# Kernel optimization log

Measured on AMD Instinct MI355X. Metric: run time of the kernel, lower is better.

Reference implementation:

```python
import jax, jax.numpy as jnp
import numpy as np
import math

B, S, D, H = 2, 2048, 1024, 16

def setup_inputs() -> dict:
    key = jax.random.key(0)
    ks = jax.random.split(key, 13)
    def lin(kw, kb, out_d, in_d):
        W = jax.random.normal(kw, (out_d, in_d), dtype=jnp.float32) * 0.02
        b = jax.random.normal(kb, (out_d,), dtype=jnp.float32) * 0.02
        return W, b
    Wq, bq = lin(ks[0], ks[1], D, D)
    Wk, bk = lin(ks[2], ks[3], D, D)
    Wv, bv = lin(ks[4], ks[5], D, D)
    Wo, bo = lin(ks[6], ks[7], D, D)
    query = jax.random.normal(ks[8], (B, S, D), dtype=jnp.float32)
    key_t = jax.random.normal(ks[9], (B, S, D), dtype=jnp.float32)
    value = jax.random.normal(ks[10], (B, S, D), dtype=jnp.float32)
    src_mask = jax.random.randint(ks[11], (B, S), 0, 2).astype(bool)  # True = masked out
    return {"query": query, "key": key_t, "value": value, "src_mask": src_mask,
            "Wq": Wq, "bq": bq, "Wk": Wk, "bk": bk, "Wv": Wv, "bv": bv,
            "Wo": Wo, "bo": bo, "nhead": H}

def reference(query, key, value, src_mask, Wq, bq, Wk, bk, Wv, bv, Wo, bo, nhead):
    b, s, d = query.shape
    hd = d // nhead
    scale = 1.0 / math.sqrt(hd)
    def split_heads(x):  # [b,s,d] -> [b,h,s,hd]
        return x.reshape(b, -1, nhead, hd).transpose(0, 2, 1, 3)
    q = split_heads(query @ Wq.T + bq)
    k = split_heads(key @ Wk.T + bk)
    v = split_heads(value @ Wv.T + bv)
    scores = jnp.einsum('bhqe,bhke->bhqk', q, k) * scale  # [b,h,s,s]
    # mask True -> -9e9, broadcast over heads and query positions (matches repeat)
    scores = jnp.where(src_mask[:, None, None, :], jnp.float32(-9e9), scores)
    probs = jax.nn.softmax(scores, axis=-1)
    # dropout is identity in eval mode
    out = jnp.einsum('bhqk,bhke->bhqe', probs, v)  # [b,h,s,hd]
    out = out.transpose(0, 2, 1, 3).reshape(b, s, d)
    out = out @ Wo.T + bo
    return out
```

## Files before the change

### kernel.cpp

```cpp
#include <hip/hip_runtime.h>
#include <hip/hip_bf16.h>
#include <cstdint>
#include <cstddef>

#define B_ 2
#define S_ 2048
#define D_ 1024
#define H_ 16
#define HD_ 64
#define M_ 4096

typedef __attribute__((ext_vector_type(8))) short short8;
typedef __attribute__((ext_vector_type(4))) float floatx4;
typedef __attribute__((ext_vector_type(16))) float f32x16;
typedef __attribute__((ext_vector_type(2))) int intx2;

__device__ __forceinline__ floatx4 mfma32(short8 a, short8 b, floatx4 c) {
    return __builtin_amdgcn_mfma_f32_16x16x32_bf16(a, b, c, 0, 0, 0);
}
__device__ __forceinline__ f32x16 mfma3216(short8 a, short8 b, f32x16 c) {
    return __builtin_amdgcn_mfma_f32_32x32x16_bf16(a, b, c, 0, 0, 0);
}

__device__ __forceinline__ void gload_lds16(const __hip_bfloat16* g, __hip_bfloat16* lds_base) {
    __builtin_amdgcn_global_load_lds(
        (const __attribute__((address_space(1))) void*)g,
        (__attribute__((address_space(3))) void*)lds_base, 16, 0, 0);
}

__device__ __forceinline__ int pkbf(float a, float b) {
    union { __hip_bfloat162 h; int i; } u;
    u.h = __float22bfloat162_rn({a, b});
    return u.i;
}
__device__ __forceinline__ void pl32swap(int& a, int& b) {
    intx2 r = __builtin_amdgcn_permlane32_swap(a, b, false, false);
    a = r.x; b = r.y;
}

__global__ __launch_bounds__(256) void cvt_all_kernel(
    const float* __restrict__ q, const float* __restrict__ k, const float* __restrict__ v,
    const float* __restrict__ wq, const float* __restrict__ wk,
    const float* __restrict__ wv, const float* __restrict__ wo,
    const int* __restrict__ mask,
    __hip_bfloat16* __restrict__ dstIn,
    __hip_bfloat16* __restrict__ dstW,
    float* __restrict__ fbias)
{
    const int bid = blockIdx.x;
    const int tid = threadIdx.x;
    const size_t SZ_IN = (size_t)M_ * D_;
    const size_t SZ_W  = (size_t)D_ * D_;
    if (bid < 12288) {
        int z = bid >> 12, xb = bid & 4095;
        const float* src = z == 0 ? q : z == 1 ? k : v;
        __hip_bfloat16* d = dstIn + (size_t)z * SZ_IN;
        int i = (xb * 256 + tid) * 4;
        float4 val = *(const float4*)(src + i);
        union { __hip_bfloat16 h[4]; uint2 u; } cv;
        cv.h[0] = __float2bfloat16(val.x); cv.h[1] = __float2bfloat16(val.y);
        cv.h[2] = __float2bfloat16(val.z); cv.h[3] = __float2bfloat16(val.w);
        *(uint2*)(d + i) = cv.u;
    } else if (bid < 16384) {
        int r  = bid - 12288;
        int z  = r >> 10, xb = r & 1023;
        const float* src = z == 0 ? wq : z == 1 ? wk : z == 2 ? wv : wo;
        __hip_bfloat16* d = dstW + (size_t)z * SZ_W;
        int i = (xb * 256 + tid) * 4;
        float4 val = *(const float4*)(src + i);
        union { __hip_bfloat16 h[4]; uint2 u; } cv;
        cv.h[0] = __float2bfloat16(val.x); cv.h[1] = __float2bfloat16(val.y);
        cv.h[2] = __float2bfloat16(val.z); cv.h[3] = __float2bfloat16(val.w);
        *(uint2*)(d + i) = cv.u;
    } else {
        int i = ((bid - 16384) * 256 + tid) * 4;
        int4 m = *(const int4*)(mask + i);
        float4 o;
        o.x = m.x ? -100000.0f : 0.0f;
        o.y = m.y ? -100000.0f : 0.0f;
        o.z = m.z ? -100000.0f : 0.0f;
        o.w = m.w ? -100000.0f : 0.0f;
        *(float4*)(fbias + i) = o;
    }
}

template <int MODE>
__device__ __forceinline__ void gemm_core(
    const __hip_bfloat16* __restrict__ A,
    const __hip_bfloat16* __restrict__ W,
    const float* __restrict__ bias,
    void* __restrict__ Cout,
    __hip_bfloat16* __restrict__ smem,
    int m0, int n0, int N)
{
    __hip_bfloat16* As = smem;
    __hip_bfloat16* Bs = smem + 128 * 32;
    const int K = D_;
    const int tid  = threadIdx.x;
    const int wave = tid >> 6;
    const int lane = tid & 63;
    const int quad = lane >> 4;
    const int l15  = lane & 15;
    const int wm   = (wave & 1) * 64;
    const int wn   = (wave >> 1) * 64;
    const int srow = lane >> 2;
    const int scol = (lane & 3) * 8;

    floatx4 acc[4][4];
#pragma unroll
    for (int i = 0; i < 4; i++)
#pragma unroll
        for (int j = 0; j < 4; j++) {
            floatx4 z = {0.f, 0.f, 0.f, 0.f};
            acc[i][j] = z;
        }

    for (int k0 = 0; k0 < K; k0 += 32) {
        __syncthreads();
#pragma unroll
        for (int t = 0; t < 2; t++) {
            int r0 = wave * 32 + t * 16;
            gload_lds16(A + (size_t)(m0 + r0 + srow) * K + k0 + scol, As + r0 * 32);
            gload_lds16(W + (size_t)(n0 + r0 + srow) * K + k0 + scol, Bs + r0 * 32);
        }
        __syncthreads();

        short8 afr[4], bfr[4];
#pragma unroll
        for (int i = 0; i < 4; i++)
            afr[i] = *(const short8*)(As + (wm + i * 16 + l15) * 32 + quad * 8);
#pragma unroll
        for (int j = 0; j < 4; j++)
            bfr[j] = *(const short8*)(Bs + (wn + j * 16 + l15) * 32 + quad * 8);
#pragma unroll
        for (int i = 0; i < 4; i++)
#pragma unroll
            for (int j = 0; j < 4; j++)
                acc[i][j] = mfma32(afr[i], bfr[j], acc[i][j]);
    }

    if constexpr (MODE == 1) {
#pragma unroll
        for (int j = 0; j < 4; j++) {
            int col = n0 + wn + j * 16 + l15;
            int h = col >> 6, e = col & 63;
            float bv = bias[col];
#pragma unroll
            for (int i = 0; i < 4; i++) {
                int s0 = m0 + wm + i * 16 + quad * 4;
                int bb = s0 >> 11, sl = s0 & 2047;
                union { __hip_bfloat16 hx[4]; uint2 u; } pk;
#pragma unroll
                for (int r = 0; r < 4; r++)
                    pk.hx[r] = __float2bfloat16(acc[i][j][r] + bv);
                *(uint2*)((__hip_bfloat16*)Cout + (((size_t)bb * H_ + h) * HD_ + e) * S_ + sl) = pk.u;
            }
        }
    } else {
#pragma unroll
        for (int j = 0; j < 4; j++) {
            int col = n0 + wn + j * 16 + l15;
            float bv = bias[col];
#pragma unroll
            for (int i = 0; i < 4; i++) {
#pragma unroll
                for (int r = 0; r < 4; r++) {
                    int rowg = m0 + wm + i * 16 + quad * 4 + r;
                    ((__hip_bfloat16*)Cout)[(size_t)rowg * N + col] =
                        __float2bfloat16(acc[i][j][r] + bv);
                }
            }
        }
    }
}

__global__ __launch_bounds__(256) void qkv_gemm_kernel(
    const __hip_bfloat16* __restrict__ qb, const __hip_bfloat16* __restrict__ kb,
    const __hip_bfloat16* __restrict__ vb,
    const __hip_bfloat16* __restrict__ Wqb, const __hip_bfloat16* __restrict__ Wkb,
    const __hip_bfloat16* __restrict__ Wvb,
    const float* __restrict__ bq, const float* __restrict__ bk, const float* __restrict__ bv,
    __hip_bfloat16* __restrict__ Qp, __hip_bfloat16* __restrict__ Kp,
    __hip_bfloat16* __restrict__ Vt)
{
    __shared__ __hip_bfloat16 smem[2 * 128 * 32] __attribute__((aligned(16)));
    const int z = blockIdx.z;
    const __hip_bfloat16* A = z == 0 ? qb : z == 1 ? kb : vb;
    const __hip_bfloat16* W = z == 0 ? Wqb : z == 1 ? Wkb : Wvb;
    const float* bias = z == 0 ? bq : z == 1 ? bk : bv;
    int m0 = blockIdx.y * 128, n0 = blockIdx.x * 128;
    if (z < 2) gemm_core<0>(A, W, bias, z == 0 ? (void*)Qp : (void*)Kp, smem, m0, n0, D_);
    else       gemm_core<1>(A, W, bias, (void*)Vt, smem, m0, n0, D_);
}

__global__ __launch_bounds__(256) void oproj_gemm_kernel(
    const __hip_bfloat16* __restrict__ A, const __hip_bfloat16* __restrict__ W,
    const float* __restrict__ bias, float* __restrict__ out)
{
    __shared__ __hip_bfloat16 As[64 * 32]  __attribute__((aligned(16)));
    __shared__ __hip_bfloat16 Bs[128 * 32] __attribute__((aligned(16)));
    const int K = D_, N = D_;
    const int tid  = threadIdx.x;
    const int m0   = blockIdx.y * 64;
    const int n0   = blockIdx.x * 128;
    const int wave = tid >> 6;
    const int lane = tid & 63;
    const int quad = lane >> 4;
    const int l15  = lane & 15;
    const int wm   = (wave & 1) * 32;
    const int wn   = (wave >> 1) * 64;
    const int srow = lane >> 2;
    const int scol = (lane & 3) * 8;

    floatx4 acc[2][4];
#pragma unroll
    for (int i = 0; i < 2; i++)
#pragma unroll
        for (int j = 0; j < 4; j++) {
            floatx4 z = {0.f, 0.f, 0.f, 0.f};
            acc[i][j] = z;
        }

    for (int k0 = 0; k0 < K; k0 += 32) {
        __syncthreads();
        {
            int ra = wave * 16;
            gload_lds16(A + (size_t)(m0 + ra + srow) * K + k0 + scol, As + ra * 32);
#pragma unroll
            for (int t = 0; t < 2; t++) {
                int rb = wave * 32 + t * 16;
                gload_lds16(W + (size_t)(n0 + rb + srow) * K + k0 + scol, Bs + rb * 32);
            }
        }
        __syncthreads();

        short8 afr[2], bfr[4];
#pragma unroll
        for (int i = 0; i < 2; i++)
            afr[i] = *(const short8*)(As + (wm + i * 16 + l15) * 32 + quad * 8);
#pragma unroll
        for (int j = 0; j < 4; j++)
            bfr[j] = *(const short8*)(Bs + (wn + j * 16 + l15) * 32 + quad * 8);
#pragma unroll
        for (int i = 0; i < 2; i++)
#pragma unroll
            for (int j = 0; j < 4; j++)
                acc[i][j] = mfma32(afr[i], bfr[j], acc[i][j]);
    }

#pragma unroll
    for (int j = 0; j < 4; j++) {
        int col = n0 + wn + j * 16 + l15;
        float bv = bias[col];
#pragma unroll
        for (int i = 0; i < 2; i++) {
#pragma unroll
            for (int r = 0; r < 4; r++) {
                int rowg = m0 + wm + i * 16 + quad * 4 + r;
                out[(size_t)rowg * N + col] = acc[i][j][r] + bv;
            }
        }
    }
}

#define LDP 72
#define NT_ (S_ / 64)
__global__ __launch_bounds__(256, 2) void flash_attn_kernel(
    const __hip_bfloat16* __restrict__ Q,
    const __hip_bfloat16* __restrict__ Kp,
    const __hip_bfloat16* __restrict__ Vt,
    const float* __restrict__ fbias,
    __hip_bfloat16* __restrict__ O)
{
    __shared__ __hip_bfloat16 Qs  [128 * LDP]    __attribute__((aligned(16)));
    __shared__ __hip_bfloat16 KsB [2][64 * LDP]  __attribute__((aligned(16)));
    __shared__ __hip_bfloat16 VtsB[2][64 * LDP]  __attribute__((aligned(16)));

    const int tid  = threadIdx.x;
    const int q0   = blockIdx.x * 128;
    const int bh   = blockIdx.y;
    const int b    = bh >> 4;
    const int h    = bh & 15;
    const int warp = tid >> 6;
    const int lane = tid & 63;
    const int l31  = lane & 31;
    const int hi   = lane >> 5;
    const float kSc = 0.18033688f;

    const size_t baseQ = ((size_t)b * S_ + q0) * D_ + (size_t)h * HD_;
#pragma unroll
    for (int c = tid; c < 1024; c += 256) {
        int row = c >> 3, kc = c & 7;
        *(uint4*)(Qs + row * LDP + kc * 8) = *(const uint4*)(Q + baseQ + (size_t)row * D_ + kc * 8);
    }

    const float* brow = fbias + b * S_;
    const __hip_bfloat16* VtBase = Vt + (size_t)bh * HD_ * S_;
    const size_t baseKrow = (size_t)b * S_ * D_ + (size_t)h * HD_;

    const int r0  = tid >> 3;
    const int kc0 = (tid & 7) * 8;

    uint4 kreg[2], vreg[2];
    auto issue = [&](int kv0) {
#pragma unroll
        for (int i = 0; i < 2; i++) {
            kreg[i] = *(const uint4*)(Kp + baseKrow + (size_t)(kv0 + r0 + 32 * i) * D_ + kc0);
            vreg[i] = *(const uint4*)(VtBase + (size_t)(r0 + 32 * i) * S_ + kv0 + kc0);
        }
    };
    auto commit = [&](int pb) {
#pragma unroll
        for (int i = 0; i < 2; i++) {
            *(uint4*)(KsB[pb]  + (r0 + 32 * i) * LDP + kc0) = kreg[i];
            *(uint4*)(VtsB[pb] + (r0 + 32 * i) * LDP + kc0) = vreg[i];
        }
    };

    issue(0);
    commit(0);
    __syncthreads();

    short8 qb[4];
#pragma unroll
    for (int ks = 0; ks < 4; ks++)
        qb[ks] = *(const short8*)(Qs + (warp * 32 + l31) * LDP + ks * 16 + hi * 8);

    float lsum = 0.f;
    f32x16 o_acc[2];
#pragma unroll
    for (int hdb = 0; hdb < 2; hdb++)
#pragma unroll
        for (int r = 0; r < 16; r++) o_acc[hdb][r] = 0.f;

    for (int t = 0; t < NT_; ++t) {
        if (t) __syncthreads();

        floatx4 brg[2][4];
#pragma unroll
        for (int kvb = 0; kvb < 2; kvb++)
#pragma unroll
            for (int g = 0; g < 4; g++)
                brg[kvb][g] = *(const floatx4*)(brow + t * 64 + kvb * 32 + g * 8 + hi * 4);

        if (t + 1 < NT_) issue((t + 1) * 64);

        const __hip_bfloat16* Ks  = KsB [t & 1];
        const __hip_bfloat16* Vts = VtsB[t & 1];

        f32x16 s_acc[2];
        __builtin_amdgcn_s_setprio(1);
#pragma unroll
        for (int kvb = 0; kvb < 2; kvb++) {
            f32x16 z;
#pragma unroll
            for (int r = 0; r < 16; r++) z[r] = 0.f;
#pragma unroll
            for (int ks = 0; ks < 4; ks++) {
                short8 ka = *(const short8*)(Ks + (kvb * 32 + l31) * LDP + ks * 16 + hi * 8);
                z = mfma3216(ka, qb[ks], z);
            }
            s_acc[kvb] = z;
        }
        __builtin_amdgcn_s_setprio(0);

        short8 pa[4];
#pragma unroll
        for (int kvb = 0; kvb < 2; kvb++) {
            float p[16];
#pragma unroll
            for (int r = 0; r < 16; r++)
                p[r] = __builtin_amdgcn_exp2f(s_acc[kvb][r] * kSc + brg[kvb][r >> 2][r & 3]);
#pragma unroll
            for (int r = 0; r < 16; r += 4)
                lsum += (p[r] + p[r + 1]) + (p[r + 2] + p[r + 3]);
#pragma unroll
            for (int ksl = 0; ksl < 2; ksl++) {
                int pb = ksl * 8;
                int w0 = pkbf(p[pb + 0], p[pb + 1]);
                int w2 = pkbf(p[pb + 4], p[pb + 5]);
                int w1 = pkbf(p[pb + 2], p[pb + 3]);
                int w3 = pkbf(p[pb + 6], p[pb + 7]);
                pl32swap(w0, w2);
                pl32swap(w1, w3);
                union { int w[4]; short8 s; } fr;
                fr.w[0] = w0; fr.w[1] = w1; fr.w[2] = w2; fr.w[3] = w3;
                pa[kvb * 2 + ksl] = fr.s;
            }
        }

        __builtin_amdgcn_s_setprio(1);
#pragma unroll
        for (int hdb = 0; hdb < 2; hdb++)
#pragma unroll
            for (int ks = 0; ks < 4; ks++) {
                short8 vb = *(const short8*)(Vts + (hdb * 32 + l31) * LDP + ks * 16 + hi * 8);
                o_acc[hdb] = mfma3216(pa[ks], vb, o_acc[hdb]);
            }
        __builtin_amdgcn_s_setprio(0);

        if (t + 1 < NT_) commit((t + 1) & 1);
    }

    lsum += __shfl_xor(lsum, 32);
    float inv = 1.0f / lsum;

    const size_t baseO = ((size_t)b * S_ + q0 + warp * 32) * D_ + (size_t)h * HD_;
#pragma unroll
    for (int r = 0; r < 16; r++) {
        int crow = (r & 3) + 8 * (r >> 2) + 4 * hi;
        float iv = __shfl(inv, crow);
#pragma unroll
        for (int hdb = 0; hdb < 2; hdb++)
            O[baseO + (size_t)crow * D_ + hdb * 32 + l31] =
                __float2bfloat16(o_acc[hdb][r] * iv);
    }
}

extern "C" void kernel_launch(void* const* d_in, const int* in_sizes, int n_in,
                              void* d_out, int out_size, void* d_ws, size_t ws_size,
                              hipStream_t stream) {
    const float* query = (const float*)d_in[0];
    const float* key   = (const float*)d_in[1];
    const float* value = (const float*)d_in[2];
    const int*   mask  = (const int*)d_in[3];
    const float* Wq    = (const float*)d_in[4];
    const float* bq    = (const float*)d_in[5];
    const float* Wk    = (const float*)d_in[6];
    const float* bk    = (const float*)d_in[7];
    const float* Wv    = (const float*)d_in[8];
    const float* bv    = (const float*)d_in[9];
    const float* Wo    = (const float*)d_in[10];
    const float* bo    = (const float*)d_in[11];
    float* out = (float*)d_out;

    const size_t SZ_IN = (size_t)M_ * D_;
    const size_t SZ_W  = (size_t)D_ * D_;
    __hip_bfloat16* qb  = (__hip_bfloat16*)d_ws;
    __hip_bfloat16* kb  = qb  + SZ_IN;
    __hip_bfloat16* vb  = kb  + SZ_IN;
    __hip_bfloat16* Wqb = vb  + SZ_IN;
    __hip_bfloat16* Wkb = Wqb + SZ_W;
    __hip_bfloat16* Wvb = Wkb + SZ_W;
    __hip_bfloat16* Wob = Wvb + SZ_W;
    __hip_bfloat16* Qp  = Wob + SZ_W;
    __hip_bfloat16* Kp  = Qp  + SZ_IN;
    __hip_bfloat16* Vt  = Kp  + SZ_IN;
    float*          fb  = (float*)(Vt + SZ_IN);

    cvt_all_kernel<<<dim3(16388), 256, 0, stream>>>(
        query, key, value, Wq, Wk, Wv, Wo, mask, qb, Wqb, fb);

    qkv_gemm_kernel<<<dim3(D_ / 128, M_ / 128, 3), 256, 0, stream>>>(
        qb, kb, vb, Wqb, Wkb, Wvb, bq, bk, bv, Qp, Kp, Vt);

    flash_attn_kernel<<<dim3(S_ / 128, B_ * H_), 256, 0, stream>>>(Qp, Kp, Vt, fb, Qp);

    oproj_gemm_kernel<<<dim3(D_ / 128, M_ / 64), 256, 0, stream>>>(Qp, Wob, bo, out);
}
```

Before: 249.4 us.

## Split each KV tile across two warp groups in flash attention

The attention kernel now runs 512 threads per block. Two groups of four warps each take one 32-key half of every 64-key tile and keep their own partial output and row-sum accumulators. The halves are combined through shared memory at the end, and the Q, K and V staging is folded into one shared buffer that is reused for that reduction. The aim is more resident waves and shorter per-warp dependency chains to hide latency. In exchange it adds an epilogue reduction, and the tighter launch bounds raise register pressure and the risk of spills.

Result: faster. 229.5 us (-8.0%).

```diff
diff --git a/kernel.cpp b/kernel.cpp
--- a/kernel.cpp
+++ b/kernel.cpp
@@ -264,17 +264,16 @@
 }
 
 #define LDP 72
-#define NT_ (S_ / 64)
-__global__ __launch_bounds__(256, 2) void flash_attn_kernel(
+#define NTK (S_ / 64)
+#define KVBUF (64 * LDP)
+__global__ __launch_bounds__(512, 4) void flash_attn_kernel(
     const __hip_bfloat16* __restrict__ Q,
     const __hip_bfloat16* __restrict__ Kp,
     const __hip_bfloat16* __restrict__ Vt,
     const float* __restrict__ fbias,
     __hip_bfloat16* __restrict__ O)
 {
-    __shared__ __hip_bfloat16 Qs  [128 * LDP]    __attribute__((aligned(16)));
-    __shared__ __hip_bfloat16 KsB [2][64 * LDP]  __attribute__((aligned(16)));
-    __shared__ __hip_bfloat16 VtsB[2][64 * LDP]  __attribute__((aligned(16)));
+    __shared__ __hip_bfloat16 smem[4 * KVBUF] __attribute__((aligned(16)));
 
     const int tid  = threadIdx.x;
     const int q0   = blockIdx.x * 128;
@@ -282,6 +281,8 @@
     const int b    = bh >> 4;
     const int h    = bh & 15;
     const int warp = tid >> 6;
+    const int qw   = warp & 3;
+    const int kvh  = warp >> 2;
     const int lane = tid & 63;
     const int l31  = lane & 31;
     const int hi   = lane >> 5;
@@ -289,10 +290,17 @@
 
     const size_t baseQ = ((size_t)b * S_ + q0) * D_ + (size_t)h * HD_;
 #pragma unroll
-    for (int c = tid; c < 1024; c += 256) {
+    for (int c = tid; c < 1024; c += 512) {
         int row = c >> 3, kc = c & 7;
-        *(uint4*)(Qs + row * LDP + kc * 8) = *(const uint4*)(Q + baseQ + (size_t)row * D_ + kc * 8);
-    }
+        *(uint4*)(smem + row * LDP + kc * 8) =
+            *(const uint4*)(Q + baseQ + (size_t)row * D_ + kc * 8);
+    }
+    __syncthreads();
+    short8 qb[4];
+#pragma unroll
+    for (int ks = 0; ks < 4; ks++)
+        qb[ks] = *(const short8*)(smem + (qw * 32 + l31) * LDP + ks * 16 + hi * 8);
+    __syncthreads();
 
     const float* brow = fbias + b * S_;
     const __hip_bfloat16* VtBase = Vt + (size_t)bh * HD_ * S_;
@@ -301,31 +309,20 @@
     const int r0  = tid >> 3;
     const int kc0 = (tid & 7) * 8;
 
-    uint4 kreg[2], vreg[2];
+    uint4 kreg, vreg;
     auto issue = [&](int kv0) {
-#pragma unroll
-        for (int i = 0; i < 2; i++) {
-            kreg[i] = *(const uint4*)(Kp + baseKrow + (size_t)(kv0 + r0 + 32 * i) * D_ + kc0);
-            vreg[i] = *(const uint4*)(VtBase + (size_t)(r0 + 32 * i) * S_ + kv0 + kc0);
-        }
+        kreg = *(const uint4*)(Kp + baseKrow + (size_t)(kv0 + r0) * D_ + kc0);
+        vreg = *(const uint4*)(VtBase + (size_t)r0 * S_ + kv0 + kc0);
     };
     auto commit = [&](int pb) {
-#pragma unroll
-        for (int i = 0; i < 2; i++) {
-            *(uint4*)(KsB[pb]  + (r0 + 32 * i) * LDP + kc0) = kreg[i];
-            *(uint4*)(VtsB[pb] + (r0 + 32 * i) * LDP + kc0) = vreg[i];
-        }
+        *(uint4*)(smem + pb * KVBUF + r0 * LDP + kc0) = kreg;
+        *(uint4*)(smem + (2 + pb) * KVBUF + r0 * LDP + kc0) = vreg;
     };
 
     issue(0);
     commit(0);
     __syncthreads();
 
-    short8 qb[4];
-#pragma unroll
-    for (int ks = 0; ks < 4; ks++)
-        qb[ks] = *(const short8*)(Qs + (warp * 32 + l31) * LDP + ks * 16 + hi * 8);
-
     float lsum = 0.f;
     f32x16 o_acc[2];
 #pragma unroll
@@ -333,87 +330,95 @@
 #pragma unroll
         for (int r = 0; r < 16; r++) o_acc[hdb][r] = 0.f;
 
-    for (int t = 0; t < NT_; ++t) {
+    for (int t = 0; t < NTK; ++t) {
         if (t) __syncthreads();
 
-        floatx4 brg[2][4];
-#pragma unroll
-        for (int kvb = 0; kvb < 2; kvb++)
-#pragma unroll
-            for (int g = 0; g < 4; g++)
-                brg[kvb][g] = *(const floatx4*)(brow + t * 64 + kvb * 32 + g * 8 + hi * 4);
-
-        if (t + 1 < NT_) issue((t + 1) * 64);
-
-        const __hip_bfloat16* Ks  = KsB [t & 1];
-        const __hip_bfloat16* Vts = VtsB[t & 1];
-
-        f32x16 s_acc[2];
+        if (t + 1 < NTK) issue((t + 1) * 64);
+
+        const __hip_bfloat16* Ks  = smem + (t & 1) * KVBUF;
+        const __hip_bfloat16* Vts = smem + (2 + (t & 1)) * KVBUF;
+
+        f32x16 z;
+#pragma unroll
+        for (int r = 0; r < 16; r++) z[r] = 0.f;
         __builtin_amdgcn_s_setprio(1);
 #pragma unroll
-        for (int kvb = 0; kvb < 2; kvb++) {
-            f32x16 z;
-#pragma unroll
-            for (int r = 0; r < 16; r++) z[r] = 0.f;
-#pragma unroll
-            for (int ks = 0; ks < 4; ks++) {
-                short8 ka = *(const short8*)(Ks + (kvb * 32 + l31) * LDP + ks * 16 + hi * 8);
-                z = mfma3216(ka, qb[ks], z);
-            }
-            s_acc[kvb] = z;
+        for (int ks = 0; ks < 4; ks++) {
+            short8 ka = *(const short8*)(Ks + (kvh * 32 + l31) * LDP + ks * 16 + hi * 8);
+            z = mfma3216(ka, qb[ks], z);
         }
         __builtin_amdgcn_s_setprio(0);
 
-        short8 pa[4];
-#pragma unroll
-        for (int kvb = 0; kvb < 2; kvb++) {
-            float p[16];
+        short8 pa[2];
+#pragma unroll
+        for (int ksl = 0; ksl < 2; ksl++) {
+            const float* bb = brow + t * 64 + kvh * 32 + ksl * 16 + hi * 4;
+            floatx4 b0 = *(const floatx4*)(bb);
+            floatx4 b1 = *(const floatx4*)(bb + 8);
+            float p[8];
+#pragma unroll
+            for (int i = 0; i < 8; i++) {
+                float bias = (i < 4) ? b0[i & 3] : b1[i & 3];
+                p[i] = __builtin_amdgcn_exp2f(z[ksl * 8 + i] * kSc + bias);
+            }
+            lsum += ((p[0] + p[1]) + (p[2] + p[3])) + ((p[4] + p[5]) + (p[6] + p[7]));
+            int w0 = pkbf(p[0], p[1]);
+            int w2 = pkbf(p[4], p[5]);
+            int w1 = pkbf(p[2], p[3]);
+            int w3 = pkbf(p[6], p[7]);
+            pl32swap(w0, w2);
+            pl32swap(w1, w3);
+            union { int w[4]; short8 s; } fr;
+            fr.w[0] = w0; fr.w[1] = w1; fr.w[2] = w2; fr.w[3] = w3;
+            pa[ksl] = fr.s;
+        }
+
+        __builtin_amdgcn_s_setprio(1);
+#pragma unroll
+        for (int hdb = 0; hdb < 2; hdb++)
+#pragma unroll
+            for (int ksl = 0; ksl < 2; ksl++) {
+                short8 vb = *(const short8*)(Vts + (hdb * 32 + l31) * LDP +
+                                             kvh * 32 + ksl * 16 + hi * 8);
+                o_acc[hdb] = mfma3216(pa[ksl], vb, o_acc[hdb]);
+            }
+        __builtin_amdgcn_s_setprio(0);
+
+        if (t + 1 < NTK) commit((t + 1) & 1);
+    }
+
+    __syncthreads();
+    float* ored = (float*)smem;
+    float* lred = (float*)smem + 8192;
+    if (kvh == 1) {
+#pragma unroll
+        for (int hdb = 0; hdb < 2; hdb++)
 #pragma unroll
             for (int r = 0; r < 16; r++)
-                p[r] = __builtin_amdgcn_exp2f(s_acc[kvb][r] * kSc + brg[kvb][r >> 2][r & 3]);
-#pragma unroll
-            for (int r = 0; r < 16; r += 4)
-                lsum += (p[r] + p[r + 1]) + (p[r + 2] + p[r + 3]);
-#pragma unroll
-            for (int ksl = 0; ksl < 2; ksl++) {
-                int pb = ksl * 8;
-                int w0 = pkbf(p[pb + 0], p[pb + 1]);
-                int w2 = pkbf(p[pb + 4], p[pb + 5]);
-                int w1 = pkbf(p[pb + 2], p[pb + 3]);
-                int w3 = pkbf(p[pb + 6], p[pb + 7]);
-                pl32swap(w0, w2);
-                pl32swap(w1, w3);
-                union { int w[4]; short8 s; } fr;
-                fr.w[0] = w0; fr.w[1] = w1; fr.w[2] = w2; fr.w[3] = w3;
-                pa[kvb * 2 + ksl] = fr.s;
-            }
-        }
-
-        __builtin_amdgcn_s_setprio(1);
+                ored[(hdb * 16 + r) * 256 + qw * 64 + lane] = o_acc[hdb][r];
+        lred[qw * 64 + lane] = lsum;
+    }
+    __syncthreads();
+    if (kvh == 0) {
 #pragma unroll
         for (int hdb = 0; hdb < 2; hdb++)
 #pragma unroll
-            for (int ks = 0; ks < 4; ks++) {
-                short8 vb = *(const short8*)(Vts + (hdb * 32 + l31) * LDP + ks * 16 + hi * 8);
-                o_acc[hdb] = mfma3216(pa[ks], vb, o_acc[hdb]);
-            }
-        __builtin_amdgcn_s_setprio(0);
-
-        if (t + 1 < NT_) commit((t + 1) & 1);
-    }
-
-    lsum += __shfl_xor(lsum, 32);
-    float inv = 1.0f / lsum;
-
-    const size_t baseO = ((size_t)b * S_ + q0 + warp * 32) * D_ + (size_t)h * HD_;
-#pragma unroll
-    for (int r = 0; r < 16; r++) {
-        int crow = (r & 3) + 8 * (r >> 2) + 4 * hi;
-        float iv = __shfl(inv, crow);
-#pragma unroll
-        for (int hdb = 0; hdb < 2; hdb++)
-            O[baseO + (size_t)crow * D_ + hdb * 32 + l31] =
-                __float2bfloat16(o_acc[hdb][r] * iv);
+            for (int r = 0; r < 16; r++)
+                o_acc[hdb][r] += ored[(hdb * 16 + r) * 256 + qw * 64 + lane];
+        float ls = lsum + lred[qw * 64 + lane];
+        ls += __shfl_xor(ls, 32);
+        float inv = 1.0f / ls;
+
+        const size_t baseO = ((size_t)b * S_ + q0 + qw * 32) * D_ + (size_t)h * HD_;
+#pragma unroll
+        for (int r = 0; r < 16; r++) {
+            int crow = (r & 3) + 8 * (r >> 2) + 4 * hi;
+            float iv = __shfl(inv, crow);
+#pragma unroll
+            for (int hdb = 0; hdb < 2; hdb++)
+                O[baseO + (size_t)crow * D_ + hdb * 32 + l31] =
+                    __float2bfloat16(o_acc[hdb][r] * iv);
+        }
     }
 }
 
@@ -454,7 +459,7 @@
     qkv_gemm_kernel<<<dim3(D_ / 128, M_ / 128, 3), 256, 0, stream>>>(
         qb, kb, vb, Wqb, Wkb, Wvb, bq, bk, bv, Qp, Kp, Vt);
 
-    flash_attn_kernel<<<dim3(S_ / 128, B_ * H_), 256, 0, stream>>>(Qp, Kp, Vt, fb, Qp);
+    flash_attn_kernel<<<dim3(S_ / 128, B_ * H_), 512, 0, stream>>>(Qp, Kp, Vt, fb, Qp);
 
     oproj_gemm_kernel<<<dim3(D_ / 128, M_ / 64), 256, 0, stream>>>(Qp, Wob, bo, out);
 }
```
